# Performance work log

Measured on AMD Instinct MI355X. Metric: run time of the kernel, lower is better.

## Reference

```python
import jax, jax.numpy as jnp
import numpy as np

EPS = 1e-5
NEG_SLOPE = 0.1


def conv2d(x, w, b, pad):
    y = jax.lax.conv_general_dilated(x, w, (1, 1), ((pad[0], pad[0]), (pad[1], pad[1])),
                                     dimension_numbers=('NCHW', 'OIHW', 'NCHW'))
    return y + b[None, :, None, None]


def bn(x, g, b, m, v):
    # inference-mode BatchNorm2d
    scale = g / jnp.sqrt(v + EPS)
    return (x - m[None, :, None, None]) * scale[None, :, None, None] + b[None, :, None, None]


def leaky(x):
    return jnp.where(x >= 0, x, NEG_SLOPE * x)


def pos_embed(C, T, V):
    # STTFormer-style sinusoidal embedding over joint index, repeated per frame
    pos = jnp.tile(jnp.arange(V, dtype=jnp.float32), T)[:, None]            # (T*V, 1)
    div = jnp.exp(jnp.arange(0, C, 2, dtype=jnp.float32) * (-np.log(10000.0) / C))
    pe = jnp.zeros((T * V, C), jnp.float32)
    pe = pe.at[:, 0::2].set(jnp.sin(pos * div)).at[:, 1::2].set(jnp.cos(pos * div))
    return pe.reshape(T, V, C).transpose(2, 0, 1)[None]                      # (1, C, T, V)


def ema(x, c1w, c1b, c3w, c3b, gng, gnb, groups):
    # Efficient Multi-scale Attention (EMA) module
    b, c, h, w = x.shape
    cg = c // groups
    gx = x.reshape(b * groups, cg, h, w)
    x_h = gx.mean(axis=3, keepdims=True)                                     # (bg, cg, h, 1)
    x_w = jnp.swapaxes(gx.mean(axis=2, keepdims=True), 2, 3)                 # (bg, cg, w, 1)
    hw = conv2d(jnp.concatenate([x_h, x_w], axis=2), c1w, c1b, (0, 0))       # 1x1 conv
    xh, xw = hw[:, :, :h], hw[:, :, h:]
    g = gx * jax.nn.sigmoid(xh) * jax.nn.sigmoid(jnp.swapaxes(xw, 2, 3))
    # GroupNorm(cg, cg): one channel per group -> per-channel spatial norm
    mu = g.mean((2, 3), keepdims=True)
    var = g.var((2, 3), keepdims=True)
    x1 = (g - mu) / jnp.sqrt(var + EPS) * gng[None, :, None, None] + gnb[None, :, None, None]
    x2 = conv2d(gx, c3w, c3b, (1, 1))                                        # 3x3 conv
    x11 = jax.nn.softmax(x1.mean((2, 3))[:, None, :], axis=-1)               # (bg, 1, cg)
    x21 = jax.nn.softmax(x2.mean((2, 3))[:, None, :], axis=-1)
    x12 = x2.reshape(b * groups, cg, h * w)
    x22 = x1.reshape(b * groups, cg, h * w)
    weights = (x11 @ x12 + x21 @ x22).reshape(b * groups, 1, h, w)
    return (gx * jax.nn.sigmoid(weights)).reshape(b, c, h, w)


def _forward(x, atten_weight, qkv_w, qkv_b, alphas, att0s, nets_w, nets_b,
             bn1_g, bn1_b, bn1_m, bn1_v,
             e1_c1w, e1_c1b, e1_c3w, e1_c3b, e1_gng, e1_gnb,
             bn2_g, bn2_b, bn2_m, bn2_v,
             nett_w, nett_b, bn3_g, bn3_b, bn3_m, bn3_v,
             e2_c1w, e2_c1b, e2_c3w, e2_c3b, e2_gng, e2_gnb,
             bn4_g, bn4_b, bn4_m, bn4_v):
    N, C, T, V = x.shape
    H = alphas.shape[1]
    D = qkv_w.shape[0] // (2 * H)
    xs = pos_embed(C, T, V) + x
    # 1x1 conv to q,k
    qk = jnp.einsum('oc,nctv->notv', qkv_w, xs) + qkv_b[None, :, None, None]
    qk = qk.reshape(N, 2 * H, D, T, V)
    q, k = qk[:, :H], qk[:, H:]
    # tanh attention over joints (V x V), scaled, weighted, plus learned bias table
    att = jnp.tanh(jnp.einsum('nhctu,nhctv->nhuv', q, k) / (D * T)) * alphas
    att = att * atten_weight[None, None] + att0s
    xs = jnp.einsum('nctu,nhuv->nhctv', x, att).reshape(N, H * C, T, V)
    x_ress = x  # in_channels == out_channels -> identity residual
    xs = leaky(bn(conv2d(xs, nets_w, nets_b, (0, 1)), bn1_g, bn1_b, bn1_m, bn1_v) + x_ress)
    xs = leaky(bn(ema(xs, e1_c1w, e1_c1b, e1_c3w, e1_c3b, e1_gng, e1_gnb, 16),
                  bn2_g, bn2_b, bn2_m, bn2_v) + x_ress)
    xt = leaky(bn(conv2d(xs, nett_w, nett_b, (2, 0)), bn3_g, bn3_b, bn3_m, bn3_v) + xs)
    xt = leaky(bn(ema(xt, e2_c1w, e2_c1b, e2_c3w, e2_c3b, e2_gng, e2_gnb, 32),
                  bn4_g, bn4_b, bn4_m, bn4_v) + xs)
    return xt


def setup_inputs() -> dict:
    key = jax.random.key(0)
    N, C, T, V, H, D, O = 64, 64, 120, 25, 3, 64, 64
    cg1, cg2 = O // 16, O // 32
    ks = jax.random.split(key, 16)
    f32 = jnp.float32

    def bn_params(k, c):
        k1, k2 = jax.random.split(k)
        return (jnp.ones(c, f32), jnp.zeros(c, f32),
                jax.random.normal(k1, (c,), f32) * 0.1,
                jax.random.uniform(k2, (c,), f32) + 0.5)

    bn1 = bn_params(ks[5], O)
    bn2 = bn_params(ks[6], O)
    bn3 = bn_params(ks[7], O)
    bn4 = bn_params(ks[8], O)
    return {
        'x': jax.random.normal(ks[0], (N, C, T, V), f32),
        'atten_weight': jax.random.uniform(ks[1], (V, V), f32),
        'qkv_w': jax.random.normal(ks[2], (2 * H * D, C), f32) * 0.05,
        'qkv_b': jnp.zeros(2 * H * D, f32),
        'alphas': jnp.ones((1, H, 1, 1), f32),
        'att0s': jnp.ones((1, H, V, V), f32) / V,
        'nets_w': jax.random.normal(ks[3], (O, C * H, 1, 3), f32) * 0.05,
        'nets_b': jnp.zeros(O, f32),
        'bn1_g': bn1[0], 'bn1_b': bn1[1], 'bn1_m': bn1[2], 'bn1_v': bn1[3],
        'e1_c1w': jax.random.normal(ks[9], (cg1, cg1, 1, 1), f32) * 0.1,
        'e1_c1b': jnp.zeros(cg1, f32),
        'e1_c3w': jax.random.normal(ks[10], (cg1, cg1, 3, 3), f32) * 0.1,
        'e1_c3b': jnp.zeros(cg1, f32),
        'e1_gng': jnp.ones(cg1, f32), 'e1_gnb': jnp.zeros(cg1, f32),
        'bn2_g': bn2[0], 'bn2_b': bn2[1], 'bn2_m': bn2[2], 'bn2_v': bn2[3],
        'nett_w': jax.random.normal(ks[4], (O, O, 5, 1), f32) * 0.05,
        'nett_b': jnp.zeros(O, f32),
        'bn3_g': bn3[0], 'bn3_b': bn3[1], 'bn3_m': bn3[2], 'bn3_v': bn3[3],
        'e2_c1w': jax.random.normal(ks[11], (cg2, cg2, 1, 1), f32) * 0.1,
        'e2_c1b': jnp.zeros(cg2, f32),
        'e2_c3w': jax.random.normal(ks[12], (cg2, cg2, 3, 3), f32) * 0.1,
        'e2_c3b': jnp.zeros(cg2, f32),
        'e2_gng': jnp.ones(cg2, f32), 'e2_gnb': jnp.zeros(cg2, f32),
        'bn4_g': bn4[0], 'bn4_b': bn4[1], 'bn4_m': bn4[2], 'bn4_v': bn4[3],
    }


def reference(x, atten_weight, qkv_w, qkv_b, alphas, att0s, nets_w, nets_b,
              bn1_g, bn1_b, bn1_m, bn1_v,
              e1_c1w, e1_c1b, e1_c3w, e1_c3b, e1_gng, e1_gnb,
              bn2_g, bn2_b, bn2_m, bn2_v,
              nett_w, nett_b, bn3_g, bn3_b, bn3_m, bn3_v,
              e2_c1w, e2_c1b, e2_c3w, e2_c3b, e2_gng, e2_gnb,
              bn4_g, bn4_b, bn4_m, bn4_v):
    return _forward(x, atten_weight, qkv_w, qkv_b, alphas, att0s, nets_w, nets_b,
                    bn1_g, bn1_b, bn1_m, bn1_v,
                    e1_c1w, e1_c1b, e1_c3w, e1_c3b, e1_gng, e1_gnb,
                    bn2_g, bn2_b, bn2_m, bn2_v,
                    nett_w, nett_b, bn3_g, bn3_b, bn3_m, bn3_v,
                    e2_c1w, e2_c1b, e2_c3w, e2_c3b, e2_gng, e2_gnb,
                    bn4_g, bn4_b, bn4_m, bn4_v)
```

## Files before the change

kernel.cpp:

```cpp
#include <hip/hip_runtime.h>

__device__ __forceinline__ float sigm(float x){ return 1.f/(1.f+__expf(-x)); }

__device__ __forceinline__ float waveReduceSum(float v){
  #pragma unroll
  for (int o = 32; o > 0; o >>= 1) v += __shfl_down(v, o, 64);
  return v;
}
__device__ __forceinline__ float blockReduceSum(float v, float* red4, int tid){
  v = waveReduceSum(v);
  __syncthreads();
  if ((tid & 63) == 0) red4[tid >> 6] = v;
  __syncthreads();
  return red4[0] + red4[1] + red4[2] + red4[3];
}

__global__ __launch_bounds__(256) void zeroS_kernel(float* __restrict__ S){
  int i = blockIdx.x*256 + threadIdx.x;
  if (i < 120000) S[i] = 0.f;
}

__global__ __launch_bounds__(256) void att_partial_kernel(
    const float* __restrict__ x, const float* __restrict__ qkv_w, const float* __restrict__ qkv_b,
    float* __restrict__ S)
{
  const int nh = blockIdx.x;
  const int tc = blockIdx.y;
  const int n = nh / 3, h = nh % 3;
  const int tid = threadIdx.x;
  __shared__ float Wq[4096], Wk[4096];
  __shared__ float pe[1600];
  __shared__ float xt[1600];
  __shared__ float Qs[1600], Ks[1600];
  __shared__ float qb[64], kb[64];
  for (int i = tid; i < 4096; i += 256){
    int cq = i & 63, c = i >> 6;
    Wq[c*64+cq] = qkv_w[(size_t)(h*64 + cq)*64 + c];
    Wk[c*64+cq] = qkv_w[(size_t)((3+h)*64 + cq)*64 + c];
  }
  if (tid < 64){ qb[tid] = qkv_b[h*64 + tid]; kb[tid] = qkv_b[(3+h)*64 + tid]; }
  for (int i = tid; i < 1600; i += 256){
    int c = i / 25, v = i % 25;
    float freq = __expf(-(float)(2*(c>>1)) * 0.14391156835f);
    float a = (float)v * freq;
    pe[i] = (c & 1) ? cosf(a) : sinf(a);
  }
  float sacc[5] = {0,0,0,0,0};
  const int u = tid / 5, v0 = (tid % 5) * 5;
  for (int t = tc*15; t < tc*15 + 15; ++t){
    __syncthreads();
    for (int i = tid; i < 1600; i += 256){
      int c = i / 25, uu = i % 25;
      xt[i] = x[((size_t)((n*64 + c)*120 + t))*25 + uu] + pe[i];
    }
    __syncthreads();
    if (tid < 160){
      int qk = tid / 80; int r = tid % 80; int cq0 = (r/5)*4; int u0 = (r%5)*5;
      const float* W = qk ? Wk : Wq;
      const float* bb = qk ? kb : qb;
      float acc[4][5];
      #pragma unroll
      for (int i=0;i<4;i++){ float b = bb[cq0+i];
        #pragma unroll
        for (int j=0;j<5;j++) acc[i][j] = b; }
      const float* Wb = &W[cq0];
      const float* xb = &xt[u0];
      #pragma unroll 8
      for (int c = 0; c < 64; ++c){
        float xv[5];
        #pragma unroll
        for (int j=0;j<5;j++) xv[j] = xb[c*25 + j];
        #pragma unroll
        for (int i=0;i<4;i++){
          float w = Wb[c*64 + i];
          #pragma unroll
          for (int j=0;j<5;j++) acc[i][j] += w * xv[j];
        }
      }
      float* Out = qk ? Ks : Qs;
      #pragma unroll
      for (int i=0;i<4;i++)
        #pragma unroll
        for (int j=0;j<5;j++) Out[(cq0+i)*25 + u0 + j] = acc[i][j];
    }
    __syncthreads();
    if (tid < 125){
      const float* Qb = &Qs[u];
      const float* Kb = &Ks[v0];
      #pragma unroll 8
      for (int c = 0; c < 64; ++c){
        float q = Qb[c*25];
        #pragma unroll
        for (int j=0;j<5;j++) sacc[j] += q * Kb[c*25 + j];
      }
    }
  }
  if (tid < 125){
    float* dst = S + (size_t)nh*625 + u*25 + v0;
    #pragma unroll
    for (int j=0;j<5;j++) atomicAdd(dst + j, sacc[j]);
  }
}

__global__ __launch_bounds__(256) void att_finalize_kernel(
    float* __restrict__ S, const float* __restrict__ attw,
    const float* __restrict__ alphas, const float* __restrict__ att0s)
{
  int idx = blockIdx.x*256 + threadIdx.x;
  if (idx >= 120000) return;
  int nh = idx / 625, uv = idx % 625;
  int h = nh % 3;
  float a = tanhf(S[idx] * (1.f/7680.f)) * alphas[h];
  S[idx] = a * attw[uv] + att0s[h*625 + uv];
}

__global__ __launch_bounds__(256) void stage1_kernel(
    const float* __restrict__ x, const float* __restrict__ att,
    const float* __restrict__ nets_w, const float* __restrict__ nets_b,
    const float* __restrict__ bng, const float* __restrict__ bnb,
    const float* __restrict__ bnm, const float* __restrict__ bnv,
    float* __restrict__ s1)
{
  __shared__ float smem[9451];
  float* sc    = smem;
  float* sh    = smem + 64;
  float* att_s = smem + 128;
  float* xts   = smem + 2003;
  float* xbp   = smem + 5267;
  float* wbuf  = smem + 7867;
  const int n = blockIdx.x, t0 = blockIdx.y*2;
  const int tid = threadIdx.x;

  for (int i=tid;i<1875;i+=256) att_s[i] = att[(size_t)n*1875 + i];
  for (int i=tid;i<3200;i+=256){
    int c=i/50, r=i%50;
    xts[c*51 + r] = x[((size_t)(n*64+c)*120 + t0 + r/25)*25 + (r%25)];
  }
  if (tid < 192){
    int row=tid>>2, p=tid&3;
    xbp[row*54 + ((p&1)?26:0) + ((p>>1)?27:0)] = 0.f;
  }
  if (tid < 64){
    float s = bng[tid]*rsqrtf(bnv[tid]+1e-5f);
    sc[tid]=s; sh[tid]=bnb[tid]-bnm[tid]*s;
  }
  __syncthreads();

  const int op = tid>>3, r = tid&7, tt = r>>2, vq = r&3;
  const int o0 = op*2, v0q = vq*7, nv = (vq<3)?7:4;
  const int w4 = tid&3, oS = tid>>2;
  const float* gw_base = nets_w + (size_t)oS*576 + w4*6;
  float*       wv_base = wbuf + w4*396 + oS*3;
  float acc[2][7] = {{0,0,0,0,0,0,0},{0,0,0,0,0,0,0}};

  for (int q=0; q<4; ++q){
    const int hc0 = q*48;
    if (tid < 240){
      int hcH = tid % 48, vg = tid / 48;
      int hc = hc0 + hcH;
      int h = hc>>6, c = hc&63, v0 = vg*5;
      float a0[5]={0,0,0,0,0}, a1[5]={0,0,0,0,0};
      const float* xr0 = &xts[c*51];
      const float* xr1 = &xts[c*51 + 25];
      for (int u=0;u<25;u++){
        float xv0 = xr0[u], xv1 = xr1[u];
        const float* ap = &att_s[(h*25+u)*25 + v0];
        #pragma unroll
        for (int j=0;j<5;j++){ float a=ap[j]; a0[j]+=xv0*a; a1[j]+=xv1*a; }
      }
      #pragma unroll
      for (int j=0;j<5;j++){
        xbp[hcH*54 + 1 + v0 + j]      = a0[j];
        xbp[hcH*54 + 27 + 1 + v0 + j] = a1[j];
      }
    }
    __syncthreads();

    for (int k=0;k<6;k++){
      const float* gsrc = gw_base + (hc0 + k*8)*3;
      #pragma unroll
      for (int j=0;j<6;j++)
        wv_base[(j/3)*198 + (j%3)] = gsrc[j];
      __syncthreads();
      const float* xbase = &xbp[k*8*54 + tt*27 + v0q];
      const float* wb    = &wbuf[o0*3];
      #pragma unroll 2
      for (int hcL=0; hcL<8; hcL++){
        float xr[9];
        #pragma unroll
        for (int j=0;j<9;j++) xr[j] = xbase[hcL*54 + j];
        float w00=wb[hcL*198+0], w01=wb[hcL*198+1], w02=wb[hcL*198+2],
              w10=wb[hcL*198+3], w11=wb[hcL*198+4], w12=wb[hcL*198+5];
        #pragma unroll
        for (int j=0;j<7;j++){
          acc[0][j] += w00*xr[j] + w01*xr[j+1] + w02*xr[j+2];
          acc[1][j] += w10*xr[j] + w11*xr[j+1] + w12*xr[j+2];
        }
      }
      __syncthreads();
    }
  }

  float b0 = nets_b[o0], b1 = nets_b[o0+1];
  const int t = t0 + tt;
  #pragma unroll
  for (int j=0;j<7;j++){
    if (j < nv){
      int v = v0q + j;
      size_t base0 = ((size_t)(n*64+o0)*120 + t)*25 + v;
      size_t base1 = ((size_t)(n*64+o0+1)*120 + t)*25 + v;
      float y0 = (acc[0][j] + b0)*sc[o0]   + sh[o0]   + x[base0];
      float y1 = (acc[1][j] + b1)*sc[o0+1] + sh[o0+1] + x[base1];
      y0 = (y0>=0.f)? y0 : 0.1f*y0;
      y1 = (y1>=0.f)? y1 : 0.1f*y1;
      s1[base0] = y0;
      s1[base1] = y1;
    }
  }
}

__global__ __launch_bounds__(256) void stage3_kernel(
    const float* __restrict__ s2, const float* __restrict__ nett_w, const float* __restrict__ nett_b,
    const float* __restrict__ bng, const float* __restrict__ bnb,
    const float* __restrict__ bnm, const float* __restrict__ bnv,
    float* __restrict__ s3)
{
  const int n = blockIdx.x, t0 = blockIdx.y*4;
  const int tid = threadIdx.x;
  __shared__ float tile[12800];
  __shared__ float sc[64], sh[64];
  for (int i=tid;i<12800;i+=256){
    int c=i/200, r=i%200, tt=r/25, v=r%25;
    int t = t0 + tt - 2;
    tile[i] = (t>=0 && t<120) ? s2[((size_t)(n*64+c)*120 + t)*25 + v] : 0.f;
  }
  if (tid < 64){
    float s = bng[tid]*rsqrtf(bnv[tid]+1e-5f);
    sc[tid]=s; sh[tid]=bnb[tid]-bnm[tid]*s;
  }
  __syncthreads();
  for (int task=tid; task<800; task+=256){
    int og = task/25, v = task%25; int o0 = og*2;
    float acc[2][4];
    #pragma unroll
    for (int i=0;i<2;i++){ float b = nett_b[o0+i];
      #pragma unroll
      for (int k=0;k<4;k++) acc[i][k]=b; }
    const float* tb = &tile[v];
    const float* wbase = nett_w + (size_t)o0*320;
    #pragma unroll 4
    for (int c=0;c<64;c++){
      float xr[8];
      #pragma unroll
      for (int k=0;k<8;k++) xr[k] = tb[c*200 + k*25];
      #pragma unroll
      for (int i=0;i<2;i++){
        float w[5];
        #pragma unroll
        for (int d=0;d<5;d++) w[d] = wbase[i*320 + c*5 + d];
        #pragma unroll
        for (int k=0;k<4;k++){
          #pragma unroll
          for (int d=0;d<5;d++) acc[i][k] += w[d]*xr[k+d];
        }
      }
    }
    #pragma unroll
    for (int i=0;i<2;i++)
      #pragma unroll
      for (int k=0;k<4;k++){
        int o=o0+i, t=t0+k;
        float r2 = tile[o*200 + (k+2)*25 + v];
        float y = acc[i][k]*sc[o] + sh[o] + r2;
        y = (y>=0.f)? y : 0.1f*y;
        s3[((size_t)(n*64+o)*120 + t)*25 + v] = y;
      }
  }
}

template<int CG, int G>
__global__ __launch_bounds__(256) void ema_kernel(
    const float* __restrict__ in, const float* __restrict__ res,
    const float* __restrict__ c1w, const float* __restrict__ c1b,
    const float* __restrict__ c3w, const float* __restrict__ c3b,
    const float* __restrict__ gng, const float* __restrict__ gnb,
    const float* __restrict__ bng, const float* __restrict__ bnb,
    const float* __restrict__ bnm, const float* __restrict__ bnv,
    float* __restrict__ out)
{
  constexpr int PR = 122*27;
  __shared__ float gx[CG*PR];
  __shared__ float xh[CG*120], xw[CG*25];
  __shared__ float sigh[CG*120], sigw[CG*25];
  __shared__ float red4[4];
  __shared__ float c1w_s[CG*CG], c1b_s[CG], c3w_s[CG*CG*9], c3b_s[CG],
                   gng_s[CG], gnb_s[CG], sc_s[CG], sh_s[CG];
  const int tid = threadIdx.x;
  const int b = blockIdx.x; const int n = b / G; const int grp = b % G; const int c0 = grp*CG;
  const float* src = in + (size_t)(n*64 + c0)*3000;
  for (int i = tid; i < CG*PR; i += 256) gx[i] = 0.f;
  if (tid < CG*CG) c1w_s[tid] = c1w[tid];
  if (tid < CG*CG*9) c3w_s[tid] = c3w[tid];
  if (tid < CG){
    c1b_s[tid] = c1b[tid];
    c3b_s[tid] = c3b[tid]; gng_s[tid]=gng[tid]; gnb_s[tid]=gnb[tid];
    float s = bng[c0+tid] * rsqrtf(bnv[c0+tid]+1e-5f);
    sc_s[tid] = s; sh_s[tid] = bnb[c0+tid] - bnm[c0+tid]*s;
  }
  __syncthreads();
  for (int i = tid; i < CG*3000; i += 256){
    int cc = i/3000, p = i%3000, t = p/25, v = p%25;
    gx[cc*PR + (t+1)*27 + (v+1)] = src[i];
  }
  __syncthreads();
  for (int j = tid; j < CG*120; j += 256){
    int cc=j/120, t=j%120; float s=0;
    for (int v=0;v<25;v++) s += gx[cc*PR+(t+1)*27+(v+1)];
    xh[j] = s*(1.f/25.f);
  }
  for (int j = tid; j < CG*25; j += 256){
    int cc=j/25, v=j%25; float s=0;
    for (int t=0;t<120;t++) s += gx[cc*PR+(t+1)*27+(v+1)];
    xw[j] = s*(1.f/120.f);
  }
  __syncthreads();
  for (int j = tid; j < CG*120; j += 256){
    int cc=j/120, t=j%120; float s=c1b_s[cc];
    #pragma unroll
    for (int i=0;i<CG;i++) s += c1w_s[cc*CG+i]*xh[i*120+t];
    sigh[j] = sigm(s);
  }
  for (int j = tid; j < CG*25; j += 256){
    int cc=j/25, v=j%25; float s=c1b_s[cc];
    #pragma unroll
    for (int i=0;i<CG;i++) s += c1w_s[cc*CG+i]*xw[i*25+v];
    sigw[j] = sigm(s);
  }
  __syncthreads();
  float gs[CG], gss[CG];
  #pragma unroll
  for (int cc=0;cc<CG;cc++){ gs[cc]=0.f; gss[cc]=0.f; }
  for (int p = tid; p < 3000; p += 256){
    int t=p/25, v=p%25;
    #pragma unroll
    for (int cc=0;cc<CG;cc++){
      float g = gx[cc*PR+(t+1)*27+(v+1)]*sigh[cc*120+t]*sigw[cc*25+v];
      gs[cc]+=g; gss[cc]+=g*g;
    }
  }
  #pragma unroll
  for (int cc=0;cc<CG;cc++){
    gs[cc]  = blockReduceSum(gs[cc],  red4, tid);
    gss[cc] = blockReduceSum(gss[cc], red4, tid);
  }
  float mu[CG], inv[CG];
  #pragma unroll
  for (int cc=0;cc<CG;cc++){
    mu[cc] = gs[cc]*(1.f/3000.f);
    float var = gss[cc]*(1.f/3000.f) - mu[cc]*mu[cc];
    inv[cc] = rsqrtf(fmaxf(var, 0.f) + 1e-5f);
  }
  float x11[CG];
  { float mx = gnb_s[0];
    #pragma unroll
    for (int cc=1;cc<CG;cc++) mx = fmaxf(mx, gnb_s[cc]);
    float sum=0;
    #pragma unroll
    for (int cc=0;cc<CG;cc++){ x11[cc]=__expf(gnb_s[cc]-mx); sum+=x11[cc]; }
    float r = 1.f/sum;
    #pragma unroll
    for (int cc=0;cc<CG;cc++) x11[cc]*=r; }
  float Sall[CG];
  #pragma unroll
  for (int i=0;i<CG;i++){ float s=0; for (int t=0;t<120;t++) s += xh[i*120+t]; Sall[i]=s*25.f; }
  float m2[CG];
  #pragma unroll
  for (int cc=0;cc<CG;cc++){
    float acc = c3b_s[cc]*3000.f;
    #pragma unroll
    for (int i=0;i<CG;i++){
      #pragma unroll
      for (int dy=0;dy<3;dy++){
        #pragma unroll
        for (int dx=0;dx<3;dx++){
          float w = c3w_s[(cc*CG+i)*9+dy*3+dx];
          float ss = Sall[i];
          int re = -1, ce = -1;
          if (dy==0){ ss -= 25.f*xh[i*120+119]; re=119; }
          else if (dy==2){ ss -= 25.f*xh[i*120+0]; re=0; }
          if (dx==0){ ss -= 120.f*xw[i*25+24]; ce=24; }
          else if (dx==2){ ss -= 120.f*xw[i*25+0]; ce=0; }
          if (re>=0 && ce>=0) ss += gx[i*PR + (re+1)*27 + (ce+1)];
          acc += w*ss;
        }
      }
    }
    m2[cc] = acc*(1.f/3000.f);
  }
  float x21[CG];
  { float mx = m2[0];
    #pragma unroll
    for (int cc=1;cc<CG;cc++) mx = fmaxf(mx, m2[cc]);
    float sum=0;
    #pragma unroll
    for (int cc=0;cc<CG;cc++){ x21[cc]=__expf(m2[cc]-mx); sum+=x21[cc]; }
    float r = 1.f/sum;
    #pragma unroll
    for (int cc=0;cc<CG;cc++) x21[cc]*=r; }
  float wm[CG*9]; float bm=0.f, kc=0.f;
  #pragma unroll
  for (int k=0;k<CG*9;k++){
    float s=0;
    #pragma unroll
    for (int cc=0;cc<CG;cc++) s += x11[cc]*c3w_s[cc*CG*9 + k];
    wm[k]=s;
  }
  float ga[CG];
  #pragma unroll
  for (int cc=0;cc<CG;cc++){
    bm += x11[cc]*c3b_s[cc];
    ga[cc] = x21[cc]*gng_s[cc]*inv[cc];
    kc += x21[cc]*(gnb_s[cc] - mu[cc]*gng_s[cc]*inv[cc]);
  }
  const float base = bm + kc;
  for (int p = tid; p < 3000; p += 256){
    int t=p/25, v=p%25;
    float wsum = base;
    #pragma unroll
    for (int i=0;i<CG;i++){
      const float* gp = &gx[i*PR + t*27 + v];
      wsum += wm[i*9+0]*gp[0]  + wm[i*9+1]*gp[1]  + wm[i*9+2]*gp[2]
            + wm[i*9+3]*gp[27] + wm[i*9+4]*gp[28] + wm[i*9+5]*gp[29]
            + wm[i*9+6]*gp[54] + wm[i*9+7]*gp[55] + wm[i*9+8]*gp[56];
    }
    #pragma unroll
    for (int cc=0;cc<CG;cc++){
      float g = gx[cc*PR+(t+1)*27+(v+1)]*sigh[cc*120+t]*sigw[cc*25+v];
      wsum += ga[cc]*g;
    }
    float sw = sigm(wsum);
    #pragma unroll
    for (int cc=0;cc<CG;cc++){
      float val = gx[cc*PR+(t+1)*27+(v+1)]*sw;
      float y = val*sc_s[cc] + sh_s[cc] + res[(size_t)(n*64+c0+cc)*3000 + p];
      y = (y >= 0.f) ? y : 0.1f*y;
      out[(size_t)(n*64+c0+cc)*3000 + p] = y;
    }
  }
}

extern "C" void kernel_launch(void* const* d_in, const int* in_sizes, int n_in,
                              void* d_out, int out_size, void* d_ws, size_t ws_size,
                              hipStream_t stream)
{
  const float* x      = (const float*)d_in[0];
  const float* attw   = (const float*)d_in[1];
  const float* qkv_w  = (const float*)d_in[2];
  const float* qkv_b  = (const float*)d_in[3];
  const float* alphas = (const float*)d_in[4];
  const float* att0s  = (const float*)d_in[5];
  const float* nets_w = (const float*)d_in[6];
  const float* nets_b = (const float*)d_in[7];
  const float* bn1g = (const float*)d_in[8];  const float* bn1b = (const float*)d_in[9];
  const float* bn1m = (const float*)d_in[10]; const float* bn1v = (const float*)d_in[11];
  const float* e1c1w = (const float*)d_in[12]; const float* e1c1b = (const float*)d_in[13];
  const float* e1c3w = (const float*)d_in[14]; const float* e1c3b = (const float*)d_in[15];
  const float* e1gng = (const float*)d_in[16]; const float* e1gnb = (const float*)d_in[17];
  const float* bn2g = (const float*)d_in[18]; const float* bn2b = (const float*)d_in[19];
  const float* bn2m = (const float*)d_in[20]; const float* bn2v = (const float*)d_in[21];
  const float* nettw = (const float*)d_in[22]; const float* nettb = (const float*)d_in[23];
  const float* bn3g = (const float*)d_in[24]; const float* bn3b = (const float*)d_in[25];
  const float* bn3m = (const float*)d_in[26]; const float* bn3v = (const float*)d_in[27];
  const float* e2c1w = (const float*)d_in[28]; const float* e2c1b = (const float*)d_in[29];
  const float* e2c3w = (const float*)d_in[30]; const float* e2c3b = (const float*)d_in[31];
  const float* e2gng = (const float*)d_in[32]; const float* e2gnb = (const float*)d_in[33];
  const float* bn4g = (const float*)d_in[34]; const float* bn4b = (const float*)d_in[35];
  const float* bn4m = (const float*)d_in[36]; const float* bn4v = (const float*)d_in[37];

  float* S    = (float*)d_ws;
  float* outf = (float*)d_out;
  float* xbuf = (float*)d_in[0];

  zeroS_kernel<<<469,256,0,stream>>>(S);
  att_partial_kernel<<<dim3(192,8),256,0,stream>>>(x, qkv_w, qkv_b, S);
  att_finalize_kernel<<<469,256,0,stream>>>(S, attw, alphas, att0s);
  stage1_kernel<<<dim3(64,60),256,0,stream>>>(x, S, nets_w, nets_b, bn1g,bn1b,bn1m,bn1v, outf);
  ema_kernel<4,16><<<1024,256,0,stream>>>(outf, x,
      e1c1w,e1c1b,e1c3w,e1c3b,e1gng,e1gnb, bn2g,bn2b,bn2m,bn2v, xbuf);
  stage3_kernel<<<dim3(64,30),256,0,stream>>>(xbuf, nettw, nettb, bn3g,bn3b,bn3m,bn3v, outf);
  ema_kernel<2,32><<<2048,256,0,stream>>>(outf, xbuf,
      e2c1w,e2c1b,e2c3w,e2c3b,e2gng,e2gnb, bn4g,bn4b,bn4m,bn4v, outf);
}
```

Measured before the change: 1.207 ms.

## Read conv weights directly from global in stage1 and keep pos-embed in registers

In stage1, the staged shared-memory weight buffer and its per-chunk barriers are removed. Each thread now loads its two output channels' weights straight from global/L1, which shrinks LDS use, and launch bounds request 4 blocks per CU for higher occupancy. In the attention partial kernel, the positional embedding and global offsets are precomputed into registers instead of a shared array, avoiding recomputed index math. The cost is more global/cache traffic for weights, since 8 threads share each pair of channels and rely on cache hits, plus extra register pressure.

```diff
diff --git a/kernel.cpp b/kernel.cpp
--- a/kernel.cpp
+++ b/kernel.cpp
@@ -29,7 +29,6 @@
   const int n = nh / 3, h = nh % 3;
   const int tid = threadIdx.x;
   __shared__ float Wq[4096], Wk[4096];
-  __shared__ float pe[1600];
   __shared__ float xt[1600];
   __shared__ float Qs[1600], Ks[1600];
   __shared__ float qb[64], kb[64];
@@ -39,19 +38,26 @@
     Wk[c*64+cq] = qkv_w[(size_t)((3+h)*64 + cq)*64 + c];
   }
   if (tid < 64){ qb[tid] = qkv_b[h*64 + tid]; kb[tid] = qkv_b[(3+h)*64 + tid]; }
-  for (int i = tid; i < 1600; i += 256){
-    int c = i / 25, v = i % 25;
-    float freq = __expf(-(float)(2*(c>>1)) * 0.14391156835f);
-    float a = (float)v * freq;
-    pe[i] = (c & 1) ? cosf(a) : sinf(a);
+  float pe_reg[7]; int goff[7];
+  #pragma unroll
+  for (int k=0;k<7;k++){
+    int i = tid + k*256;
+    if (i < 1600){
+      int c = i/25, uu = i%25;
+      float freq = __expf(-(float)(2*(c>>1)) * 0.14391156835f);
+      float a = (float)uu * freq;
+      pe_reg[k] = (c & 1) ? cosf(a) : sinf(a);
+      goff[k] = (n*64 + c)*3000 + uu;
+    }
   }
   float sacc[5] = {0,0,0,0,0};
   const int u = tid / 5, v0 = (tid % 5) * 5;
   for (int t = tc*15; t < tc*15 + 15; ++t){
     __syncthreads();
-    for (int i = tid; i < 1600; i += 256){
-      int c = i / 25, uu = i % 25;
-      xt[i] = x[((size_t)((n*64 + c)*120 + t))*25 + uu] + pe[i];
+    #pragma unroll
+    for (int k=0;k<7;k++){
+      int i = tid + k*256;
+      if (i < 1600) xt[i] = x[goff[k] + t*25] + pe_reg[k];
     }
     __syncthreads();
     if (tid < 160){
@@ -114,20 +120,19 @@
   S[idx] = a * attw[uv] + att0s[h*625 + uv];
 }
 
-__global__ __launch_bounds__(256) void stage1_kernel(
+__global__ __launch_bounds__(256,4) void stage1_kernel(
     const float* __restrict__ x, const float* __restrict__ att,
     const float* __restrict__ nets_w, const float* __restrict__ nets_b,
     const float* __restrict__ bng, const float* __restrict__ bnb,
     const float* __restrict__ bnm, const float* __restrict__ bnv,
     float* __restrict__ s1)
 {
-  __shared__ float smem[9451];
+  __shared__ float smem[7872];
   float* sc    = smem;
   float* sh    = smem + 64;
   float* att_s = smem + 128;
   float* xts   = smem + 2003;
   float* xbp   = smem + 5267;
-  float* wbuf  = smem + 7867;
   const int n = blockIdx.x, t0 = blockIdx.y*2;
   const int tid = threadIdx.x;
 
@@ -148,9 +153,6 @@
 
   const int op = tid>>3, r = tid&7, tt = r>>2, vq = r&3;
   const int o0 = op*2, v0q = vq*7, nv = (vq<3)?7:4;
-  const int w4 = tid&3, oS = tid>>2;
-  const float* gw_base = nets_w + (size_t)oS*576 + w4*6;
-  float*       wv_base = wbuf + w4*396 + oS*3;
   float acc[2][7] = {{0,0,0,0,0,0,0},{0,0,0,0,0,0,0}};
 
   for (int q=0; q<4; ++q){
@@ -176,29 +178,23 @@
     }
     __syncthreads();
 
-    for (int k=0;k<6;k++){
-      const float* gsrc = gw_base + (hc0 + k*8)*3;
-      #pragma unroll
-      for (int j=0;j<6;j++)
-        wv_base[(j/3)*198 + (j%3)] = gsrc[j];
-      __syncthreads();
-      const float* xbase = &xbp[k*8*54 + tt*27 + v0q];
-      const float* wb    = &wbuf[o0*3];
-      #pragma unroll 2
-      for (int hcL=0; hcL<8; hcL++){
-        float xr[9];
-        #pragma unroll
-        for (int j=0;j<9;j++) xr[j] = xbase[hcL*54 + j];
-        float w00=wb[hcL*198+0], w01=wb[hcL*198+1], w02=wb[hcL*198+2],
-              w10=wb[hcL*198+3], w11=wb[hcL*198+4], w12=wb[hcL*198+5];
-        #pragma unroll
-        for (int j=0;j<7;j++){
-          acc[0][j] += w00*xr[j] + w01*xr[j+1] + w02*xr[j+2];
-          acc[1][j] += w10*xr[j] + w11*xr[j+1] + w12*xr[j+2];
-        }
-      }
-      __syncthreads();
-    }
+    const float* xbase = &xbp[tt*27 + v0q];
+    const float* wg0 = nets_w + (size_t)o0*576 + hc0*3;
+    const float* wg1 = wg0 + 576;
+    #pragma unroll 4
+    for (int hcL=0; hcL<48; ++hcL){
+      float xr[9];
+      #pragma unroll
+      for (int j=0;j<9;j++) xr[j] = xbase[hcL*54 + j];
+      float w00=wg0[hcL*3+0], w01=wg0[hcL*3+1], w02=wg0[hcL*3+2];
+      float w10=wg1[hcL*3+0], w11=wg1[hcL*3+1], w12=wg1[hcL*3+2];
+      #pragma unroll
+      for (int j=0;j<7;j++){
+        acc[0][j] += w00*xr[j] + w01*xr[j+1] + w02*xr[j+2];
+        acc[1][j] += w10*xr[j] + w11*xr[j+1] + w12*xr[j+2];
+      }
+    }
+    __syncthreads();
   }
 
   float b0 = nets_b[o0], b1 = nets_b[o0+1];
```

Result: faster. 1.095 ms (-9.3%).
